# Performance work log

Measured on AMD Instinct MI355X. Metric: run time of the kernel, lower is better.

Reference implementation:

```python
import jax, jax.numpy as jnp
import numpy as np

B, L, D, H, E, K = 1, 512, 512, 512, 32, 2

def setup_inputs() -> dict:
    key = jax.random.key(0)
    ks = jax.random.split(key, 6)
    x = jax.random.normal(ks[0], (B, L, D), dtype=jnp.float32)
    router_scale = 1.0 + 0.02 * jax.random.normal(ks[1], (D,), dtype=jnp.float32)
    router_logits_w = 0.02 * jax.random.normal(ks[2], (D, E), dtype=jnp.float32)
    gating_einsum = 0.02 * jax.random.normal(ks[3], (E, 2, H, D), dtype=jnp.float32)
    linear_w = 0.02 * jax.random.normal(ks[4], (E, H, D), dtype=jnp.float32)
    per_expert_scale = 1.0 + 0.02 * jax.random.normal(ks[5], (E,), dtype=jnp.float32)
    return {"x": x, "router_scale": router_scale, "router_logits_w": router_logits_w,
            "gating_einsum": gating_einsum, "linear_w": linear_w,
            "per_expert_scale": per_expert_scale}

def reference(x, router_scale, router_logits_w, gating_einsum, linear_w, per_expert_scale):
    d = x.shape[-1]
    n_experts = router_logits_w.shape[-1]
    # RMSNorm without scale (fp32)
    x32 = x.astype(jnp.float32)
    var = jnp.mean(jnp.square(x32), axis=-1, keepdims=True)
    router_input = x32 * jax.lax.rsqrt(var + 1e-6)
    root_size = jax.lax.rsqrt(jnp.asarray(d, dtype=router_input.dtype))
    router_input = router_input * root_size * router_scale.astype(router_input.dtype)
    logits = jnp.dot(router_input, router_logits_w).astype(jnp.float32)  # [B,L,E]
    probs = jax.nn.softmax(logits, axis=-1)
    _, top_k_indices = jax.lax.top_k(logits, K)  # [B,L,K]
    indicator = jax.nn.one_hot(top_k_indices, n_experts, dtype=probs.dtype).sum(axis=-2)
    gate_weights = indicator * probs
    renorm = jnp.sum(gate_weights, axis=-1, keepdims=True)
    renorm = jnp.where(renorm > 0.0, renorm, 1.0)
    weights = probs / renorm
    top_k_weights = jnp.take_along_axis(weights, top_k_indices, axis=-1)  # [B,L,K]
    output = jnp.zeros_like(x)
    for ki in range(K):  # small fixed k; faithful to source's per-slot gather
        expert_idx = top_k_indices[:, :, ki]          # [B,L] int32
        expert_w = top_k_weights[:, :, ki]            # [B,L]
        gate_params = gating_einsum[expert_idx]       # [B,L,2,H,D] -- the big gather
        lin_params = linear_w[expert_idx]             # [B,L,H,D]
        escale = per_expert_scale[expert_idx]         # [B,L]
        gate_0 = jnp.einsum('bld,blhd->blh', x, gate_params[:, :, 0])
        gate_1 = jnp.einsum('bld,blhd->blh', x, gate_params[:, :, 1])
        activated = jax.nn.gelu(gate_0) * gate_1
        expert_out = jnp.einsum('blh,blhd->bld', activated, lin_params)
        output = output + expert_out * (escale * expert_w)[..., None]
    return output
```

## Files before the change

### kernel.cpp

```cpp
#include <hip/hip_runtime.h>
#include <hip/hip_bf16.h>
#include <math.h>

#define LTOK 512
#define DDIM 512
#define NEXP 32
#define HDIM 512

typedef __attribute__((ext_vector_type(8))) short short8;
typedef __attribute__((ext_vector_type(4))) float floatx4;

__device__ __forceinline__ unsigned bpack(float a, float b) {
    unsigned ua = __float_as_uint(a), ub = __float_as_uint(b);
    ua += 0x7FFFu + ((ua >> 16) & 1u);
    ub += 0x7FFFu + ((ub >> 16) & 1u);
    return (ua >> 16) | (ub & 0xFFFF0000u);
}

__device__ __forceinline__ void stage16(const float* g, void* l) {
    __builtin_amdgcn_global_load_lds(
        (const __attribute__((address_space(1))) void*)g,
        (__attribute__((address_space(3))) void*)l, 16, 0, 0);
}
__device__ __forceinline__ void stage4(const float* g, void* l) {
    __builtin_amdgcn_global_load_lds(
        (const __attribute__((address_space(1))) void*)g,
        (__attribute__((address_space(3))) void*)l, 4, 0, 0);
}


__global__ __launch_bounds__(64) void router_kernel(
    const float* __restrict__ x, const float* __restrict__ rs,
    const float* __restrict__ Wr, const float* __restrict__ pes,
    int* __restrict__ easgn, float* __restrict__ wts,
    short* __restrict__ xb, float* __restrict__ out)
{
    const int t = blockIdx.x;
    const int lane = threadIdx.x;

    float xv[8];
    float ss = 0.f;
#pragma unroll
    for (int j = 0; j < 8; ++j) {
        xv[j] = x[t * DDIM + j * 64 + lane];
        ss += xv[j] * xv[j];
    }
#pragma unroll
    for (int j = 0; j < 8; ++j) {
        xb[t * DDIM + j * 64 + lane] = (short)(bpack(xv[j], 0.f) & 0xFFFFu);
        out[t * DDIM + j * 64 + lane] = 0.f;
    }

#pragma unroll
    for (int o = 32; o > 0; o >>= 1) ss += __shfl_xor(ss, o);
    const float var = ss * (1.0f / 512.0f);
    const float coef = rsqrtf(var + 1e-6f) * rsqrtf(512.0f);

    __shared__ float ri[DDIM];
#pragma unroll
    for (int j = 0; j < 8; ++j) {
        const int d = j * 64 + lane;
        ri[d] = xv[j] * coef * rs[d];
    }
    __syncthreads();

    const int e = lane & 31;
    const int half = lane >> 5;
    const int dbeg = half * 256;
    float l0 = 0.f, l1 = 0.f, l2 = 0.f, l3 = 0.f;
#pragma unroll 4
    for (int d = dbeg; d < dbeg + 256; d += 4) {
        l0 = fmaf(ri[d + 0], Wr[(d + 0) * NEXP + e], l0);
        l1 = fmaf(ri[d + 1], Wr[(d + 1) * NEXP + e], l1);
        l2 = fmaf(ri[d + 2], Wr[(d + 2) * NEXP + e], l2);
        l3 = fmaf(ri[d + 3], Wr[(d + 3) * NEXP + e], l3);
    }
    float lg = (l0 + l1) + (l2 + l3);
    lg += __shfl_xor(lg, 32);

    __shared__ float lgs[NEXP];
    if (lane < 32) lgs[lane] = lg;
    __syncthreads();

    if (lane == 0) {
        int i0 = 0; float m0 = lgs[0];
        for (int i = 1; i < NEXP; ++i) if (lgs[i] > m0) { m0 = lgs[i]; i0 = i; }
        int i1 = -1; float m1 = -1e30f;
        for (int i = 0; i < NEXP; ++i) if (i != i0 && lgs[i] > m1) { m1 = lgs[i]; i1 = i; }
        const float e1 = expf(m1 - m0);
        const float inv = 1.0f / (1.0f + e1);
        easgn[2 * t]     = i0;
        easgn[2 * t + 1] = i1;
        wts[2 * t]     = inv * pes[i0];
        wts[2 * t + 1] = e1 * inv * pes[i1];
    }
}

__global__ __launch_bounds__(256, 2) void gates_kernel(
    const short* __restrict__ xb, const float* __restrict__ G,
    const int* __restrict__ easgn, short* __restrict__ act)
{
    const int e  = blockIdx.y;
    const int h0 = blockIdx.x * 16;
    const int tid = threadIdx.x;
    const int wv   = tid >> 6;
    const int g    = wv & 1;
    const int kh   = wv >> 1;
    const int lane = tid & 63;
    const int n    = lane & 15;
    const int quad = lane >> 4;

    __shared__ __align__(16) char smem[65536];
    float (*red)[2][4][64] = (float(*)[2][4][64])smem;
    int* toks = (int*)(smem + 8192);
    int* lcnt = (int*)(smem + 8192 + 2048);

    const int4 eg = ((const int4*)easgn)[tid];

    const float* Gl = G + ((size_t)((e * 2 + g) * HDIM) + h0 + n) * DDIM + kh * 256 + quad * 8;
    char* const swv = smem + wv * 16384;
#pragma unroll
    for (int ks = 0; ks < 8; ++ks) {
#pragma unroll
        for (int half = 0; half < 2; ++half)
            stage16(Gl + ks * 32 + half * 4, swv + (ks * 2 + half) * 1024);
    }

    __builtin_amdgcn_s_waitcnt(0x0f70);
    short8 Bg[8];
#pragma unroll
    for (int ks = 0; ks < 8; ++ks) {
        const floatx4 u0 = *(const floatx4*)(swv + ks * 2048 + lane * 16);
        const floatx4 u1 = *(const floatx4*)(swv + ks * 2048 + 1024 + lane * 16);
        union { short8 s; unsigned u[4]; } B;
        B.u[0] = bpack(u0.x, u0.y);
        B.u[1] = bpack(u0.z, u0.w);
        B.u[2] = bpack(u1.x, u1.y);
        B.u[3] = bpack(u1.z, u1.w);
        Bg[ks] = B.s;
    }
    __syncthreads();

    if (tid == 0) *lcnt = 0;
    __syncthreads();
    if (eg.x == e) { int p = atomicAdd(lcnt, 1); toks[p] = 4 * tid; }
    if (eg.y == e) { int p = atomicAdd(lcnt, 1); toks[p] = 4 * tid + 1; }
    if (eg.z == e) { int p = atomicAdd(lcnt, 1); toks[p] = 4 * tid + 2; }
    if (eg.w == e) { int p = atomicAdd(lcnt, 1); toks[p] = 4 * tid + 3; }
    __syncthreads();
    const int Ne = *lcnt;
    if (Ne == 0) return;

    const short* xbh = xb + kh * 256;

    for (int mb = 0; mb < Ne; mb += 32) {
        int arow[2];
#pragma unroll
        for (int i = 0; i < 2; ++i) {
            int s = mb + i * 16 + n;
            arow[i] = toks[s < Ne ? s : Ne - 1] >> 1;
        }
        floatx4 acc[2] = {};
#pragma unroll
        for (int ks = 0; ks < 8; ++ks) {
            const int ko = ks * 32 + quad * 8;
#pragma unroll
            for (int i = 0; i < 2; ++i) {
                const short8 A = *(const short8*)(xbh + (size_t)arow[i] * DDIM + ko);
                acc[i] = __builtin_amdgcn_mfma_f32_16x16x32_bf16(A, Bg[ks], acc[i], 0, 0, 0);
            }
        }
#pragma unroll
        for (int i = 0; i < 2; ++i)
#pragma unroll
            for (int r = 0; r < 4; ++r)
                red[wv][i][r][lane] = acc[i][r];
        __syncthreads();

        {
            const int i = wv & 1;
            const int u = wv >> 1;
#pragma unroll
            for (int rr = 0; rr < 2; ++rr) {
                const int r = u * 2 + rr;
                const int s = mb + i * 16 + quad * 4 + r;
                if (s < Ne) {
                    const int a = toks[s];
                    const float g0 = red[0][i][r][lane] + red[2][i][r][lane];
                    const float g1 = red[1][i][r][lane] + red[3][i][r][lane];
                    const float uu = 0.7978845608f * (g0 + 0.044715f * g0 * g0 * g0);
                    const float sg = 1.0f / (1.0f + __expf(-2.0f * uu));
                    const float v = g0 * sg * g1;
                    act[(size_t)a * HDIM + h0 + n] = (short)(bpack(v, 0.f) & 0xFFFFu);
                }
            }
        }
        __syncthreads();
    }
}

__global__ __launch_bounds__(256, 2) void linear_kernel(
    const short* __restrict__ act, const float* __restrict__ Wl,
    const int* __restrict__ easgn, const float* __restrict__ wts,
    float* __restrict__ out)
{
    const int e  = blockIdx.y;
    const int d0 = blockIdx.x * 16;
    const int tid = threadIdx.x;
    const int wv   = tid >> 6;
    const int lane = tid & 63;
    const int n    = lane & 15;
    const int quad = lane >> 4;

    __shared__ __align__(16) float stage[4][2048];
    __shared__ float red[4][2][4][64];
    __shared__ int   toks[LTOK];
    __shared__ float wsl[LTOK];
    __shared__ int   lcnt;

    const int4 eg = ((const int4*)easgn)[tid];

    const float* Wbase = Wl + ((size_t)e * HDIM + wv * 128 + quad * 8) * DDIM + d0 + n;
#pragma unroll
    for (int ks = 0; ks < 4; ++ks) {
#pragma unroll
        for (int j = 0; j < 8; ++j)
            stage4(Wbase + (size_t)(ks * 32 + j) * DDIM, (char*)&stage[wv][0] + (ks * 8 + j) * 256);
    }

    __builtin_amdgcn_s_waitcnt(0x0f70);
    short8 Bl[4];
#pragma unroll
    for (int ks = 0; ks < 4; ++ks) {
        float w[8];
#pragma unroll
        for (int j = 0; j < 8; ++j)
            w[j] = stage[wv][(ks * 8 + j) * 64 + lane];
        union { short8 s; unsigned u[4]; } B;
        B.u[0] = bpack(w[0], w[1]);
        B.u[1] = bpack(w[2], w[3]);
        B.u[2] = bpack(w[4], w[5]);
        B.u[3] = bpack(w[6], w[7]);
        Bl[ks] = B.s;
    }

    if (tid == 0) lcnt = 0;
    __syncthreads();
    if (eg.x == e) { int p = atomicAdd(&lcnt, 1); toks[p] = 4 * tid;     wsl[p] = wts[4 * tid]; }
    if (eg.y == e) { int p = atomicAdd(&lcnt, 1); toks[p] = 4 * tid + 1; wsl[p] = wts[4 * tid + 1]; }
    if (eg.z == e) { int p = atomicAdd(&lcnt, 1); toks[p] = 4 * tid + 2; wsl[p] = wts[4 * tid + 2]; }
    if (eg.w == e) { int p = atomicAdd(&lcnt, 1); toks[p] = 4 * tid + 3; wsl[p] = wts[4 * tid + 3]; }
    __syncthreads();
    const int Ne = lcnt;
    if (Ne == 0) return;

    for (int mb = 0; mb < Ne; mb += 32) {
        int arow[2];
#pragma unroll
        for (int i = 0; i < 2; ++i) {
            int s = mb + i * 16 + n;
            arow[i] = toks[s < Ne ? s : Ne - 1];
        }
        floatx4 acc[2] = {};
#pragma unroll
        for (int ks = 0; ks < 4; ++ks) {
            const int ko = wv * 128 + ks * 32 + quad * 8;
#pragma unroll
            for (int i = 0; i < 2; ++i) {
                const short8 A = *(const short8*)(act + (size_t)arow[i] * HDIM + ko);
                acc[i] = __builtin_amdgcn_mfma_f32_16x16x32_bf16(A, Bl[ks], acc[i], 0, 0, 0);
            }
        }
#pragma unroll
        for (int i = 0; i < 2; ++i)
#pragma unroll
            for (int r = 0; r < 4; ++r)
                red[wv][i][r][lane] = acc[i][r];
        __syncthreads();

        {
            const int i = wv & 1;
            const int u = wv >> 1;
#pragma unroll
            for (int rr = 0; rr < 2; ++rr) {
                const int r = u * 2 + rr;
                const int s = mb + i * 16 + quad * 4 + r;
                if (s < Ne) {
                    const int slot = toks[s];
                    const float v = ((red[0][i][r][lane] + red[1][i][r][lane]) +
                                     (red[2][i][r][lane] + red[3][i][r][lane])) * wsl[s];
                    atomicAdd(&out[(size_t)(slot >> 1) * DDIM + d0 + n], v);
                }
            }
        }
        __syncthreads();
    }
}

extern "C" void kernel_launch(void* const* d_in, const int* in_sizes, int n_in,
                              void* d_out, int out_size, void* d_ws, size_t ws_size,
                              hipStream_t stream)
{
    const float* x   = (const float*)d_in[0];
    const float* rs  = (const float*)d_in[1];
    const float* Wr  = (const float*)d_in[2];
    const float* G   = (const float*)d_in[3];
    const float* Wl  = (const float*)d_in[4];
    const float* pes = (const float*)d_in[5];
    float* out = (float*)d_out;

    char* ws = (char*)d_ws;
    int*   easgn = (int*)(ws);
    float* wts   = (float*)(ws + 4096);
    short* xb    = (short*)(ws + 8192);
    short* act   = (short*)(ws + 532480);

    router_kernel<<<dim3(LTOK), dim3(64), 0, stream>>>(x, rs, Wr, pes, easgn, wts, xb, out);
    gates_kernel<<<dim3(32, NEXP), dim3(256), 0, stream>>>(xb, G, easgn, act);
    linear_kernel<<<dim3(32, NEXP), dim3(256), 0, stream>>>(act, Wl, easgn, wts, out);
}
```

Measured before the change: 159.2 us.

## Overlap token bucketing with weight staging and widen router blocks

```diff
diff --git a/kernel.cpp b/kernel.cpp
--- a/kernel.cpp
+++ b/kernel.cpp
@@ -28,61 +28,78 @@
         (__attribute__((address_space(3))) void*)l, 4, 0, 0);
 }
 
-
-__global__ __launch_bounds__(64) void router_kernel(
+#define RAW_BARRIER() do { \
+    asm volatile("s_waitcnt lgkmcnt(0)" ::: "memory"); \
+    __builtin_amdgcn_s_barrier(); \
+} while (0)
+
+
+__global__ __launch_bounds__(256) void router_kernel(
     const float* __restrict__ x, const float* __restrict__ rs,
     const float* __restrict__ Wr, const float* __restrict__ pes,
     int* __restrict__ easgn, float* __restrict__ wts,
     short* __restrict__ xb, float* __restrict__ out)
 {
     const int t = blockIdx.x;
-    const int lane = threadIdx.x;
-
-    float xv[8];
+    const int tid = threadIdx.x;
+    const int lane = tid & 63;
+    const int wv = tid >> 6;
+
+    float xv[2];
     float ss = 0.f;
 #pragma unroll
-    for (int j = 0; j < 8; ++j) {
-        xv[j] = x[t * DDIM + j * 64 + lane];
+    for (int j = 0; j < 2; ++j) {
+        xv[j] = x[t * DDIM + j * 256 + tid];
         ss += xv[j] * xv[j];
     }
 #pragma unroll
-    for (int j = 0; j < 8; ++j) {
-        xb[t * DDIM + j * 64 + lane] = (short)(bpack(xv[j], 0.f) & 0xFFFFu);
-        out[t * DDIM + j * 64 + lane] = 0.f;
+    for (int j = 0; j < 2; ++j) {
+        xb[t * DDIM + j * 256 + tid] = (short)(bpack(xv[j], 0.f) & 0xFFFFu);
+        out[t * DDIM + j * 256 + tid] = 0.f;
     }
 
 #pragma unroll
     for (int o = 32; o > 0; o >>= 1) ss += __shfl_xor(ss, o);
+    __shared__ float sred[4];
+    if (lane == 0) sred[wv] = ss;
+    __syncthreads();
+    ss = (sred[0] + sred[1]) + (sred[2] + sred[3]);
     const float var = ss * (1.0f / 512.0f);
     const float coef = rsqrtf(var + 1e-6f) * rsqrtf(512.0f);
 
     __shared__ float ri[DDIM];
 #pragma unroll
-    for (int j = 0; j < 8; ++j) {
-        const int d = j * 64 + lane;
+    for (int j = 0; j < 2; ++j) {
+        const int d = j * 256 + tid;
         ri[d] = xv[j] * coef * rs[d];
     }
     __syncthreads();
 
-    const int e = lane & 31;
-    const int half = lane >> 5;
-    const int dbeg = half * 256;
+    const int e = tid & 31;
+    const int seg = tid >> 5;
+    const int dbeg = seg * 64;
     float l0 = 0.f, l1 = 0.f, l2 = 0.f, l3 = 0.f;
 #pragma unroll 4
-    for (int d = dbeg; d < dbeg + 256; d += 4) {
+    for (int d = dbeg; d < dbeg + 64; d += 4) {
         l0 = fmaf(ri[d + 0], Wr[(d + 0) * NEXP + e], l0);
         l1 = fmaf(ri[d + 1], Wr[(d + 1) * NEXP + e], l1);
         l2 = fmaf(ri[d + 2], Wr[(d + 2) * NEXP + e], l2);
         l3 = fmaf(ri[d + 3], Wr[(d + 3) * NEXP + e], l3);
     }
-    float lg = (l0 + l1) + (l2 + l3);
-    lg += __shfl_xor(lg, 32);
+    __shared__ float lpart[8][NEXP];
+    lpart[seg][e] = (l0 + l1) + (l2 + l3);
+    __syncthreads();
 
     __shared__ float lgs[NEXP];
-    if (lane < 32) lgs[lane] = lg;
-    __syncthreads();
-
-    if (lane == 0) {
+    if (tid < NEXP) {
+        float v = 0.f;
+#pragma unroll
+        for (int s = 0; s < 8; ++s) v += lpart[s][tid];
+        lgs[tid] = v;
+    }
+    __syncthreads();
+
+    if (tid == 0) {
         int i0 = 0; float m0 = lgs[0];
         for (int i = 1; i < NEXP; ++i) if (lgs[i] > m0) { m0 = lgs[i]; i0 = i; }
         int i1 = -1; float m1 = -1e30f;
@@ -112,8 +129,8 @@
 
     __shared__ __align__(16) char smem[65536];
     float (*red)[2][4][64] = (float(*)[2][4][64])smem;
-    int* toks = (int*)(smem + 8192);
-    int* lcnt = (int*)(smem + 8192 + 2048);
+    __shared__ int toks[LTOK];
+    __shared__ int lcnt;
 
     const int4 eg = ((const int4*)easgn)[tid];
 
@@ -126,10 +143,21 @@
             stage16(Gl + ks * 32 + half * 4, swv + (ks * 2 + half) * 1024);
     }
 
-    __builtin_amdgcn_s_waitcnt(0x0f70);
+    if (tid == 0) lcnt = 0;
+    RAW_BARRIER();
+    if (eg.x == e) { int p = atomicAdd(&lcnt, 1); toks[p] = 4 * tid; }
+    if (eg.y == e) { int p = atomicAdd(&lcnt, 1); toks[p] = 4 * tid + 1; }
+    if (eg.z == e) { int p = atomicAdd(&lcnt, 1); toks[p] = 4 * tid + 2; }
+    if (eg.w == e) { int p = atomicAdd(&lcnt, 1); toks[p] = 4 * tid + 3; }
+    RAW_BARRIER();
+    const int Ne = lcnt;
+    if (Ne == 0) { __builtin_amdgcn_s_waitcnt(0x0f70); return; }
+
     short8 Bg[8];
-#pragma unroll
-    for (int ks = 0; ks < 8; ++ks) {
+    __builtin_amdgcn_s_waitcnt(0x0f78);
+    __builtin_amdgcn_sched_barrier(0);
+#pragma unroll
+    for (int ks = 0; ks < 4; ++ks) {
         const floatx4 u0 = *(const floatx4*)(swv + ks * 2048 + lane * 16);
         const floatx4 u1 = *(const floatx4*)(swv + ks * 2048 + 1024 + lane * 16);
         union { short8 s; unsigned u[4]; } B;
@@ -139,17 +167,20 @@
         B.u[3] = bpack(u1.z, u1.w);
         Bg[ks] = B.s;
     }
-    __syncthreads();
-
-    if (tid == 0) *lcnt = 0;
-    __syncthreads();
-    if (eg.x == e) { int p = atomicAdd(lcnt, 1); toks[p] = 4 * tid; }
-    if (eg.y == e) { int p = atomicAdd(lcnt, 1); toks[p] = 4 * tid + 1; }
-    if (eg.z == e) { int p = atomicAdd(lcnt, 1); toks[p] = 4 * tid + 2; }
-    if (eg.w == e) { int p = atomicAdd(lcnt, 1); toks[p] = 4 * tid + 3; }
-    __syncthreads();
-    const int Ne = *lcnt;
-    if (Ne == 0) return;
+    __builtin_amdgcn_s_waitcnt(0x0f70);
+    __builtin_amdgcn_sched_barrier(0);
+#pragma unroll
+    for (int ks = 4; ks < 8; ++ks) {
+        const floatx4 u0 = *(const floatx4*)(swv + ks * 2048 + lane * 16);
+        const floatx4 u1 = *(const floatx4*)(swv + ks * 2048 + 1024 + lane * 16);
+        union { short8 s; unsigned u[4]; } B;
+        B.u[0] = bpack(u0.x, u0.y);
+        B.u[1] = bpack(u0.z, u0.w);
+        B.u[2] = bpack(u1.x, u1.y);
+        B.u[3] = bpack(u1.z, u1.w);
+        Bg[ks] = B.s;
+    }
+    __syncthreads();
 
     const short* xbh = xb + kh * 256;
 
@@ -219,6 +250,7 @@
     __shared__ int   lcnt;
 
     const int4 eg = ((const int4*)easgn)[tid];
+    const float4 wt4 = ((const float4*)wts)[tid];
 
     const float* Wbase = Wl + ((size_t)e * HDIM + wv * 128 + quad * 8) * DDIM + d0 + n;
 #pragma unroll
@@ -228,10 +260,21 @@
             stage4(Wbase + (size_t)(ks * 32 + j) * DDIM, (char*)&stage[wv][0] + (ks * 8 + j) * 256);
     }
 
-    __builtin_amdgcn_s_waitcnt(0x0f70);
+    if (tid == 0) lcnt = 0;
+    RAW_BARRIER();
+    if (eg.x == e) { int p = atomicAdd(&lcnt, 1); toks[p] = 4 * tid;     wsl[p] = wt4.x; }
+    if (eg.y == e) { int p = atomicAdd(&lcnt, 1); toks[p] = 4 * tid + 1; wsl[p] = wt4.y; }
+    if (eg.z == e) { int p = atomicAdd(&lcnt, 1); toks[p] = 4 * tid + 2; wsl[p] = wt4.z; }
+    if (eg.w == e) { int p = atomicAdd(&lcnt, 1); toks[p] = 4 * tid + 3; wsl[p] = wt4.w; }
+    RAW_BARRIER();
+    const int Ne = lcnt;
+    if (Ne == 0) { __builtin_amdgcn_s_waitcnt(0x0f70); return; }
+
     short8 Bl[4];
-#pragma unroll
-    for (int ks = 0; ks < 4; ++ks) {
+    __builtin_amdgcn_s_waitcnt(0x4f70);
+    __builtin_amdgcn_sched_barrier(0);
+#pragma unroll
+    for (int ks = 0; ks < 2; ++ks) {
         float w[8];
 #pragma unroll
         for (int j = 0; j < 8; ++j)
@@ -243,16 +286,21 @@
         B.u[3] = bpack(w[6], w[7]);
         Bl[ks] = B.s;
     }
-
-    if (tid == 0) lcnt = 0;
-    __syncthreads();
-    if (eg.x == e) { int p = atomicAdd(&lcnt, 1); toks[p] = 4 * tid;     wsl[p] = wts[4 * tid]; }
-    if (eg.y == e) { int p = atomicAdd(&lcnt, 1); toks[p] = 4 * tid + 1; wsl[p] = wts[4 * tid + 1]; }
-    if (eg.z == e) { int p = atomicAdd(&lcnt, 1); toks[p] = 4 * tid + 2; wsl[p] = wts[4 * tid + 2]; }
-    if (eg.w == e) { int p = atomicAdd(&lcnt, 1); toks[p] = 4 * tid + 3; wsl[p] = wts[4 * tid + 3]; }
-    __syncthreads();
-    const int Ne = lcnt;
-    if (Ne == 0) return;
+    __builtin_amdgcn_s_waitcnt(0x0f70);
+    __builtin_amdgcn_sched_barrier(0);
+#pragma unroll
+    for (int ks = 2; ks < 4; ++ks) {
+        float w[8];
+#pragma unroll
+        for (int j = 0; j < 8; ++j)
+            w[j] = stage[wv][(ks * 8 + j) * 64 + lane];
+        union { short8 s; unsigned u[4]; } B;
+        B.u[0] = bpack(w[0], w[1]);
+        B.u[1] = bpack(w[2], w[3]);
+        B.u[2] = bpack(w[4], w[5]);
+        B.u[3] = bpack(w[6], w[7]);
+        Bl[ks] = B.s;
+    }
 
     for (int mb = 0; mb < Ne; mb += 32) {
         int arow[2];
@@ -315,7 +363,7 @@
     short* xb    = (short*)(ws + 8192);
     short* act   = (short*)(ws + 532480);
 
-    router_kernel<<<dim3(LTOK), dim3(64), 0, stream>>>(x, rs, Wr, pes, easgn, wts, xb, out);
+    router_kernel<<<dim3(LTOK), dim3(256), 0, stream>>>(x, rs, Wr, pes, easgn, wts, xb, out);
     gates_kernel<<<dim3(32, NEXP), dim3(256), 0, stream>>>(xb, G, easgn, act);
     linear_kernel<<<dim3(32, NEXP), dim3(256), 0, stream>>>(act, Wl, easgn, wts, out);
 }
```

Result: faster. 152.7 us (-4.1%).
